# Performance work log

Measured on AMD Instinct MI355X. Metric: run time of the kernel, lower is better.

## Reference

```python
import jax, jax.numpy as jnp
import numpy as np


def _gcn_conv(x, src, dst, W, b, n_nodes):
    # PyG GCNConv: add self-loops, symmetric deg^{-1/2} normalization, then linear.
    xw = x @ W  # [N, H]
    # degree including self-loop (count of incoming edges at dst + 1)
    deg = jnp.zeros((n_nodes,), dtype=xw.dtype).at[dst].add(1.0) + 1.0
    dinv = jax.lax.rsqrt(deg)  # deg >= 1 always
    coef = (dinv[src] * dinv[dst])[:, None]  # [E, 1]
    out = jnp.zeros_like(xw).at[dst].add(xw[src] * coef)
    # self-loop edge i->i has norm dinv[i]^2
    out = out + xw * (dinv * dinv)[:, None]
    return out + b


def setup_inputs() -> dict:
    key = jax.random.key(0)
    ks = jax.random.split(key, 6)
    N, E, F, H, G = 200000, 600000, 128, 128, 64
    x = jax.random.normal(ks[0], (N, F), dtype=jnp.float32)
    edge_index = jax.random.randint(ks[1], (2, E), 0, N, dtype=jnp.int64)
    batch = jnp.sort(jax.random.randint(ks[2], (N,), 0, G, dtype=jnp.int64))
    W1 = jax.random.normal(ks[3], (F, H), dtype=jnp.float32) * (1.0 / np.sqrt(F))
    b1 = jnp.zeros((H,), dtype=jnp.float32)
    W2 = jax.random.normal(ks[4], (H, H), dtype=jnp.float32) * (1.0 / np.sqrt(H))
    b2 = jnp.zeros((H,), dtype=jnp.float32)
    return {"x": x, "edge_index": edge_index, "batch": batch, "num_graphs": G,
            "W1": W1, "b1": b1, "W2": W2, "b2": b2}


def reference(x, edge_index, batch, num_graphs, W1, b1, W2, b2):
    n_nodes = x.shape[0]
    # feature standardization (torch .std is unbiased, ddof=1)
    x = (x - x.mean(axis=0, keepdims=True)) / x.std(axis=0, keepdims=True, ddof=1)
    src, dst = edge_index[0], edge_index[1]
    h = jax.nn.relu(_gcn_conv(x, src, dst, W1, b1, n_nodes))
    # dropout p=0 -> identity
    h = jax.nn.relu(_gcn_conv(h, src, dst, W2, b2, n_nodes))
    # global_add_pool over batch ids
    return jax.ops.segment_sum(h, batch, num_segments=num_graphs)
```

## Files before the change

### kernel.cpp

```cpp
#include <hip/hip_runtime.h>

#define FDIM 128

typedef __attribute__((ext_vector_type(8))) short short8;
typedef __attribute__((ext_vector_type(4))) float f32x4;

__device__ inline unsigned short f2bf(float f) {
    unsigned int u = __float_as_uint(f);
    unsigned int r = u + 0x7FFFu + ((u >> 16) & 1u);
    return (unsigned short)(r >> 16);
}
__device__ inline float bf2f(unsigned short b) {
    return __uint_as_float((unsigned int)b << 16);
}
__device__ inline void bf8_fma(short8 v, float c, float* acc) {
#pragma unroll
    for (int k = 0; k < 8; ++k)
        acc[k] = fmaf(bf2f(((const unsigned short*)&v)[k]), c, acc[k]);
}

__global__ __launch_bounds__(256) void pre_combo(const float* __restrict__ x, int N,
                                                 float* __restrict__ partials, int statBlocks,
                                                 const int* __restrict__ dst, int E,
                                                 int* __restrict__ cnt) {
    if ((int)blockIdx.x >= statBlocks) {
        int e = (blockIdx.x - statBlocks) * 256 + threadIdx.x;
        if (e < E) atomicAdd(&cnt[dst[e]], 1);
        return;
    }
    const int c4 = threadIdx.x & 31;
    const int rg = threadIdx.x >> 5;
    float4 s = make_float4(0.f, 0.f, 0.f, 0.f);
    float4 q = make_float4(0.f, 0.f, 0.f, 0.f);
    for (long r = (long)blockIdx.x * 8 + rg; r < N; r += (long)statBlocks * 8) {
        float4 v = ((const float4*)x)[r * 32 + c4];
        s.x += v.x; s.y += v.y; s.z += v.z; s.w += v.w;
        q.x += v.x * v.x; q.y += v.y * v.y; q.z += v.z * v.z; q.w += v.w * v.w;
    }
    __shared__ float red[8][32][8];
    float* p = red[rg][c4];
    p[0] = s.x; p[1] = s.y; p[2] = s.z; p[3] = s.w;
    p[4] = q.x; p[5] = q.y; p[6] = q.z; p[7] = q.w;
    __syncthreads();
    if (rg == 0) {
#pragma unroll
        for (int g = 1; g < 8; ++g) {
            const float* o = red[g][c4];
#pragma unroll
            for (int j = 0; j < 8; ++j) red[0][c4][j] += o[j];
        }
        const float* r0 = red[0][c4];
        float* out = &partials[(size_t)blockIdx.x * 256];
        ((float4*)out)[c4] = make_float4(r0[0], r0[1], r0[2], r0[3]);
        ((float4*)(out + 128))[c4] = make_float4(r0[4], r0[5], r0[6], r0[7]);
    }
}

__global__ __launch_bounds__(256) void mid_combo(const int* __restrict__ cnt, int N,
                                                 int* __restrict__ start,
                                                 int* __restrict__ wcur,
                                                 int* __restrict__ counter,
                                                 float* __restrict__ dinv,
                                                 const float* __restrict__ partials,
                                                 int nblk, int offsBlocks,
                                                 const float* __restrict__ W1,
                                                 const float* __restrict__ W2,
                                                 unsigned short* __restrict__ WT1,
                                                 unsigned short* __restrict__ WT2,
                                                 float* __restrict__ bias0) {
    const int tid = threadIdx.x;
    if ((int)blockIdx.x < offsBlocks) {
        __shared__ int sh[256];
        __shared__ int base;
        int i = blockIdx.x * 256 + tid;
        int v = (i < N) ? cnt[i] : 0;
        sh[tid] = v;
        __syncthreads();
        for (int off = 1; off < 256; off <<= 1) {
            int t = (tid >= off) ? sh[tid - off] : 0;
            __syncthreads();
            sh[tid] += t;
            __syncthreads();
        }
        if (tid == 255) base = atomicAdd(counter, sh[255]);
        __syncthreads();
        int excl = base + sh[tid] - v;
        if (i < N) {
            start[i] = excl;
            wcur[i] = excl;
            dinv[i] = rsqrtf((float)v + 1.0f);
        }
        return;
    }
    const int b = blockIdx.x - offsBlocks;
    const int h = tid & 127;
    const int seg = tid >> 7;
    if (b < 8) {
        __shared__ float red[32][32];
        __shared__ float scol[32], mean_sh[16], rstd_sh[16];
        const int rg = tid >> 3;
        const int f = tid & 7;
        const int colbase = (f < 4) ? (b * 16 + f * 4) : (128 + b * 16 + (f - 4) * 4);
        float4 a = make_float4(0.f, 0.f, 0.f, 0.f);
        for (int row = rg; row < nblk; row += 32) {
            float4 v = *(const float4*)&partials[(size_t)row * 256 + colbase];
            a.x += v.x; a.y += v.y; a.z += v.z; a.w += v.w;
        }
        *(float4*)&red[rg][f * 4] = a;
        __syncthreads();
        if (tid < 32) {
            float s = 0.f;
#pragma unroll
            for (int r = 0; r < 32; ++r) s += red[r][tid];
            scol[tid] = s;
        }
        __syncthreads();
        if (tid < 16) {
            float m = scol[tid] / (float)N;
            float var = (scol[16 + tid] - (float)N * m * m) / (float)(N - 1);
            mean_sh[tid] = m;
            rstd_sh[tid] = rsqrtf(var);
        }
        __syncthreads();
        float acc = 0.f;
#pragma unroll
        for (int jj = 0; jj < 8; ++jj) {
            int jl = seg * 8 + jj;
            int j2 = b * 16 + jl;
            float w = W1[j2 * FDIM + h] * rstd_sh[jl];
            WT1[h * FDIM + j2] = f2bf(w);
            acc += mean_sh[jl] * w;
        }
        unsafeAtomicAdd(&bias0[h], -acc);
    } else {
#pragma unroll
        for (int jj = 0; jj < 8; ++jj) {
            int j2 = (b - 8) * 16 + seg * 8 + jj;
            WT2[h * FDIM + j2] = f2bf(W2[j2 * FDIM + h]);
        }
    }
}

__global__ __launch_bounds__(256, 4) void gemm1_fill(const float* __restrict__ A,
                                                     const unsigned short* __restrict__ WT,
                                                     const float* __restrict__ bias,
                                                     unsigned short* __restrict__ C, int M,
                                                     int gemmBlocks,
                                                     const int* __restrict__ src,
                                                     const int* __restrict__ dst,
                                                     const float* __restrict__ dinv,
                                                     int* __restrict__ wcur,
                                                     int2* __restrict__ edata, int E) {
    const int tid = threadIdx.x;
    if ((int)blockIdx.x >= gemmBlocks) {
        int e = (blockIdx.x - gemmBlocks) * 256 + tid;
        if (e < E) {
            int s = src[e], d = dst[e];
            int pos = atomicAdd(&wcur[d], 1);
            edata[pos] = make_int2(s, __float_as_int(dinv[s] * dinv[d]));
        }
        return;
    }
    constexpr int LDA = 136;
    __shared__ unsigned short Alds[64 * LDA];
    const int row0 = blockIdx.x * 64;

    for (int i = tid; i < 64 * 32; i += 256) {
        int r = i >> 5, c4 = i & 31;
        int row = row0 + r;
        float4 v = make_float4(0.f, 0.f, 0.f, 0.f);
        if (row < M) v = ((const float4*)A)[(size_t)row * 32 + c4];
        ushort4 p;
        p.x = f2bf(v.x); p.y = f2bf(v.y); p.z = f2bf(v.z); p.w = f2bf(v.w);
        *(ushort4*)&Alds[r * LDA + c4 * 4] = p;
    }
    __syncthreads();

    const int lane = tid & 63;
    const int wave = tid >> 6;
    const int m16 = lane & 15;
    const int quad = lane >> 4;

    f32x4 acc[8];
#pragma unroll
    for (int t = 0; t < 8; ++t) acc[t] = (f32x4){0.f, 0.f, 0.f, 0.f};

    const unsigned short* Abase = &Alds[(wave * 16 + m16) * LDA + quad * 8];
    const unsigned short* Wg = &WT[(size_t)m16 * FDIM + quad * 8];
#pragma unroll
    for (int s = 0; s < 4; ++s) {
        short8 a = *(const short8*)&Abase[s * 32];
#pragma unroll
        for (int t = 0; t < 8; ++t) {
            short8 b = *(const short8*)&Wg[t * 16 * FDIM + s * 32];
            acc[t] = __builtin_amdgcn_mfma_f32_16x16x32_bf16(b, a, acc[t], 0, 0, 0);
        }
    }

    const int r = row0 + wave * 16 + m16;
    if (r < M) {
#pragma unroll
        for (int t = 0; t < 8; ++t) {
            ushort4 o;
            o.x = f2bf(acc[t][0] + bias[t * 16 + quad * 4 + 0]);
            o.y = f2bf(acc[t][1] + bias[t * 16 + quad * 4 + 1]);
            o.z = f2bf(acc[t][2] + bias[t * 16 + quad * 4 + 2]);
            o.w = f2bf(acc[t][3] + bias[t * 16 + quad * 4 + 3]);
            *(ushort4*)&C[(size_t)r * FDIM + t * 16 + quad * 4] = o;
        }
    }
}

__global__ __launch_bounds__(256) void agg_gemm2(const unsigned short* __restrict__ xw,
                                                 const float* __restrict__ dinv,
                                                 const int* __restrict__ start,
                                                 const int* __restrict__ cnt,
                                                 const int2* __restrict__ edata,
                                                 const float* __restrict__ bvec,
                                                 const unsigned short* __restrict__ WT2,
                                                 unsigned short* __restrict__ out,
                                                 int N) {
    const int base = blockIdx.x * 16;
    const int node = base + (threadIdx.x >> 4);
    const int l8 = threadIdx.x & 15;
    const bool active = node < N;
    const int nidx = active ? node : (N - 1);

    float dv = dinv[nidx];
    float d2 = dv * dv;
    float4 b0 = ((const float4*)bvec)[l8 * 2];
    float4 b1v = ((const float4*)bvec)[l8 * 2 + 1];
    float acc[8] = {b0.x, b0.y, b0.z, b0.w, b1v.x, b1v.y, b1v.z, b1v.w};
    short8 sv = *(const short8*)&xw[(size_t)nidx * FDIM + l8 * 8];
    bf8_fma(sv, d2, acc);

    int j = start[nidx];
    const int s1 = j + (active ? cnt[nidx] : 0);
    for (; j + 4 <= s1; j += 4) {
        int2 e0 = edata[j], e1 = edata[j + 1], e2 = edata[j + 2], e3 = edata[j + 3];
        short8 u0 = *(const short8*)&xw[(size_t)e0.x * FDIM + l8 * 8];
        short8 u1 = *(const short8*)&xw[(size_t)e1.x * FDIM + l8 * 8];
        short8 u2 = *(const short8*)&xw[(size_t)e2.x * FDIM + l8 * 8];
        short8 u3 = *(const short8*)&xw[(size_t)e3.x * FDIM + l8 * 8];
        bf8_fma(u0, __int_as_float(e0.y), acc);
        bf8_fma(u1, __int_as_float(e1.y), acc);
        bf8_fma(u2, __int_as_float(e2.y), acc);
        bf8_fma(u3, __int_as_float(e3.y), acc);
    }
    for (; j < s1; ++j) {
        int2 ed = edata[j];
        short8 u = *(const short8*)&xw[(size_t)ed.x * FDIM + l8 * 8];
        bf8_fma(u, __int_as_float(ed.y), acc);
    }

    constexpr int LDH = 136;
    __shared__ unsigned short hlds[16 * LDH];
    {
        ushort4 o0, o1;
        if (active) {
            o0.x = f2bf(fmaxf(acc[0], 0.f)); o0.y = f2bf(fmaxf(acc[1], 0.f));
            o0.z = f2bf(fmaxf(acc[2], 0.f)); o0.w = f2bf(fmaxf(acc[3], 0.f));
            o1.x = f2bf(fmaxf(acc[4], 0.f)); o1.y = f2bf(fmaxf(acc[5], 0.f));
            o1.z = f2bf(fmaxf(acc[6], 0.f)); o1.w = f2bf(fmaxf(acc[7], 0.f));
        } else {
            o0.x = 0; o0.y = 0; o0.z = 0; o0.w = 0;
            o1.x = 0; o1.y = 0; o1.z = 0; o1.w = 0;
        }
        unsigned short* hp = &hlds[(threadIdx.x >> 4) * LDH + l8 * 8];
        *(ushort4*)hp = o0;
        *(ushort4*)(hp + 4) = o1;
    }
    __syncthreads();

    const int lane = threadIdx.x & 63;
    const int wave = threadIdx.x >> 6;
    const int m16 = lane & 15;
    const int quad = lane >> 4;
    f32x4 c0 = (f32x4){0.f, 0.f, 0.f, 0.f};
    f32x4 c1 = (f32x4){0.f, 0.f, 0.f, 0.f};
    const unsigned short* Abase = &hlds[m16 * LDH + quad * 8];
    const unsigned short* Wg = &WT2[(size_t)(wave * 32 + m16) * FDIM + quad * 8];
#pragma unroll
    for (int s = 0; s < 4; ++s) {
        short8 a = *(const short8*)&Abase[s * 32];
        short8 w0 = *(const short8*)&Wg[s * 32];
        short8 w1 = *(const short8*)&Wg[16 * FDIM + s * 32];
        c0 = __builtin_amdgcn_mfma_f32_16x16x32_bf16(w0, a, c0, 0, 0, 0);
        c1 = __builtin_amdgcn_mfma_f32_16x16x32_bf16(w1, a, c1, 0, 0, 0);
    }
    const int r = base + m16;
    if (r < N) {
        ushort4 o;
        o.x = f2bf(c0[0]); o.y = f2bf(c0[1]); o.z = f2bf(c0[2]); o.w = f2bf(c0[3]);
        *(ushort4*)&out[(size_t)r * FDIM + wave * 32 + quad * 4] = o;
        o.x = f2bf(c1[0]); o.y = f2bf(c1[1]); o.z = f2bf(c1[2]); o.w = f2bf(c1[3]);
        *(ushort4*)&out[(size_t)r * FDIM + wave * 32 + 16 + quad * 4] = o;
    }
}

template <bool POOL>
__global__ __launch_bounds__(256) void aggregate(const unsigned short* __restrict__ xw,
                                                 const float* __restrict__ dinv,
                                                 const int* __restrict__ start,
                                                 const int* __restrict__ cnt,
                                                 const int2* __restrict__ edata,
                                                 const float* __restrict__ bvec,
                                                 unsigned short* __restrict__ out,
                                                 const int* __restrict__ batch,
                                                 float* __restrict__ pool_part,
                                                 int* __restrict__ ptag,
                                                 float* __restrict__ pooled, int N) {
    const int base = blockIdx.x * 16;
    const int node = base + (threadIdx.x >> 4);
    const int l8 = threadIdx.x & 15;
    const bool active = node < N;
    if (!POOL && !active) return;
    const int nidx = active ? node : (N - 1);

    float dv = dinv[nidx];
    float d2 = dv * dv;
    float4 b0 = ((const float4*)bvec)[l8 * 2];
    float4 b1 = ((const float4*)bvec)[l8 * 2 + 1];
    float acc[8] = {b0.x, b0.y, b0.z, b0.w, b1.x, b1.y, b1.z, b1.w};
    short8 sv = *(const short8*)&xw[(size_t)nidx * FDIM + l8 * 8];
    bf8_fma(sv, d2, acc);

    int j = start[nidx];
    const int s1 = j + (active ? cnt[nidx] : 0);
    for (; j + 4 <= s1; j += 4) {
        int2 e0 = edata[j], e1 = edata[j + 1], e2 = edata[j + 2], e3 = edata[j + 3];
        short8 u0 = *(const short8*)&xw[(size_t)e0.x * FDIM + l8 * 8];
        short8 u1 = *(const short8*)&xw[(size_t)e1.x * FDIM + l8 * 8];
        short8 u2 = *(const short8*)&xw[(size_t)e2.x * FDIM + l8 * 8];
        short8 u3 = *(const short8*)&xw[(size_t)e3.x * FDIM + l8 * 8];
        bf8_fma(u0, __int_as_float(e0.y), acc);
        bf8_fma(u1, __int_as_float(e1.y), acc);
        bf8_fma(u2, __int_as_float(e2.y), acc);
        bf8_fma(u3, __int_as_float(e3.y), acc);
    }
    for (; j < s1; ++j) {
        int2 ed = edata[j];
        short8 u = *(const short8*)&xw[(size_t)ed.x * FDIM + l8 * 8];
        bf8_fma(u, __int_as_float(ed.y), acc);
    }

    if constexpr (!POOL) {
        short8 o;
#pragma unroll
        for (int k = 0; k < 8; ++k)
            ((unsigned short*)&o)[k] = f2bf(fmaxf(acc[k], 0.f));
        *(short8*)&out[(size_t)node * FDIM + l8 * 8] = o;
    } else {
        float r[8];
#pragma unroll
        for (int k = 0; k < 8; ++k) r[k] = active ? fmaxf(acc[k], 0.f) : 0.f;
        int g0 = batch[base];
        int g1 = batch[min(base + 15, N - 1)];
        if (g0 == g1) {
            __shared__ float red[16][FDIM];
            float* dst = &red[threadIdx.x >> 4][l8 * 8];
            *(float4*)dst = make_float4(r[0], r[1], r[2], r[3]);
            *(float4*)(dst + 4) = make_float4(r[4], r[5], r[6], r[7]);
            __syncthreads();
            if (threadIdx.x < FDIM) {
                float s = 0.f;
#pragma unroll
                for (int i = 0; i < 16; ++i) s += red[i][threadIdx.x];
                pool_part[(size_t)blockIdx.x * FDIM + threadIdx.x] = s;
                if (threadIdx.x == 0) ptag[blockIdx.x] = g0;
            }
        } else {
            if (threadIdx.x == 0) ptag[blockIdx.x] = -1;
            if (active) {
                int g = batch[node];
#pragma unroll
                for (int k = 0; k < 8; ++k)
                    unsafeAtomicAdd(&pooled[g * FDIM + l8 * 8 + k], r[k]);
            }
        }
    }
}

__global__ __launch_bounds__(128) void pool_reduce(const float* __restrict__ pool_part,
                                                   const int* __restrict__ ptag,
                                                   int nslots, float* __restrict__ out) {
    int per = (nslots + gridDim.x - 1) / gridDim.x;
    int s0 = blockIdx.x * per;
    int s1 = min(s0 + per, nslots);
    int t = threadIdx.x;
    float acc = 0.f;
    int cur = -1;
    for (int s = s0; s < s1; ++s) {
        int g = ptag[s];
        if (g < 0) continue;
        if (g != cur) {
            if (cur >= 0) unsafeAtomicAdd(&out[cur * FDIM + t], acc);
            acc = 0.f;
            cur = g;
        }
        acc += pool_part[(size_t)s * FDIM + t];
    }
    if (cur >= 0) unsafeAtomicAdd(&out[cur * FDIM + t], acc);
}

extern "C" void kernel_launch(void* const* d_in, const int* in_sizes, int n_in,
                              void* d_out, int out_size, void* d_ws, size_t ws_size,
                              hipStream_t stream) {
    const float* x = (const float*)d_in[0];
    const int* ei = (const int*)d_in[1];
    const int* batch = (const int*)d_in[2];
    const float* W1 = (const float*)d_in[4];
    const float* b1 = (const float*)d_in[5];
    const float* W2 = (const float*)d_in[6];
    const float* b2 = (const float*)d_in[7];

    const int N = in_sizes[2];
    const int E = in_sizes[1] / 2;
    const int* srcp = ei;
    const int* dstp = ei + E;

    const size_t NF = (size_t)N * FDIM;
    const int aggGrid = (N + 15) / 16;
    unsigned short* bufA = (unsigned short*)d_ws;
    unsigned short* bufB = bufA + NF;
    int* cnt = (int*)(bufB + NF);
    int* counter = cnt + N;
    float* bias0 = (float*)(counter + 4);
    float* dinv = bias0 + FDIM;
    int* start = (int*)(dinv + N);
    int* wcur = start + N;
    unsigned short* WT1 = (unsigned short*)(wcur + N);
    unsigned short* WT2 = WT1 + FDIM * FDIM;
    int2* edata = (int2*)(WT2 + FDIM * FDIM);
    float* pool_part = (float*)(edata + E);
    int* ptag = (int*)(pool_part + (size_t)aggGrid * FDIM);
    float* partials = (float*)edata;
    const int STAT_BLOCKS = 512;

    hipMemsetAsync(cnt, 0, ((size_t)N + 4 + FDIM) * sizeof(int), stream);
    hipMemsetAsync(d_out, 0, (size_t)out_size * sizeof(float), stream);

    const int degBlocks = (E + 255) / 256;
    const int offsBlocks = (N + 255) / 256;
    const int gemmGrid = (N + 63) / 64;

    pre_combo<<<STAT_BLOCKS + degBlocks, 256, 0, stream>>>(x, N, partials, STAT_BLOCKS,
                                                           dstp, E, cnt);
    mid_combo<<<offsBlocks + 16, 256, 0, stream>>>(cnt, N, start, wcur, counter, dinv,
                                                   partials, STAT_BLOCKS, offsBlocks,
                                                   W1, W2, WT1, WT2, bias0);

    gemm1_fill<<<gemmGrid + degBlocks, 256, 0, stream>>>(x, WT1, bias0, bufA, N, gemmGrid,
                                                         srcp, dstp, dinv, wcur, edata, E);

    agg_gemm2<<<aggGrid, 256, 0, stream>>>(bufA, dinv, start, cnt, edata, b1, WT2,
                                           bufB, N);

    aggregate<true><<<aggGrid, 256, 0, stream>>>(bufB, dinv, start, cnt, edata, b2,
                                                 nullptr, batch, pool_part, ptag,
                                                 (float*)d_out, N);
    pool_reduce<<<256, 128, 0, stream>>>(pool_part, ptag, aggGrid, (float*)d_out);
}
```

Measured before the change: 433.6 us.

## Emit bf16 copy of x in stats pass and stage weights in LDS for GEMM1

The statistics kernel now writes a bf16 copy of x as it reads it, so the first GEMM reads half the bytes instead of re-reading fp32 x. GEMM1 also stages the transposed weight matrix into shared memory rather than loading B fragments from global memory, and drops the occupancy hint in launch bounds. This trades an extra 51 MB write in the stats pass plus roughly 50 KB of LDS per block (lower occupancy) for a smaller read in GEMM1 and on-chip weight reuse.

```diff
diff --git a/kernel.cpp b/kernel.cpp
--- a/kernel.cpp
+++ b/kernel.cpp
@@ -22,7 +22,8 @@
 __global__ __launch_bounds__(256) void pre_combo(const float* __restrict__ x, int N,
                                                  float* __restrict__ partials, int statBlocks,
                                                  const int* __restrict__ dst, int E,
-                                                 int* __restrict__ cnt) {
+                                                 int* __restrict__ cnt,
+                                                 unsigned short* __restrict__ xbf) {
     if ((int)blockIdx.x >= statBlocks) {
         int e = (blockIdx.x - statBlocks) * 256 + threadIdx.x;
         if (e < E) atomicAdd(&cnt[dst[e]], 1);
@@ -36,6 +37,9 @@
         float4 v = ((const float4*)x)[r * 32 + c4];
         s.x += v.x; s.y += v.y; s.z += v.z; s.w += v.w;
         q.x += v.x * v.x; q.y += v.y * v.y; q.z += v.z * v.z; q.w += v.w * v.w;
+        ushort4 p;
+        p.x = f2bf(v.x); p.y = f2bf(v.y); p.z = f2bf(v.z); p.w = f2bf(v.w);
+        ((ushort4*)xbf)[r * 32 + c4] = p;
     }
     __shared__ float red[8][32][8];
     float* p = red[rg][c4];
@@ -141,16 +145,16 @@
     }
 }
 
-__global__ __launch_bounds__(256, 4) void gemm1_fill(const float* __restrict__ A,
-                                                     const unsigned short* __restrict__ WT,
-                                                     const float* __restrict__ bias,
-                                                     unsigned short* __restrict__ C, int M,
-                                                     int gemmBlocks,
-                                                     const int* __restrict__ src,
-                                                     const int* __restrict__ dst,
-                                                     const float* __restrict__ dinv,
-                                                     int* __restrict__ wcur,
-                                                     int2* __restrict__ edata, int E) {
+__global__ __launch_bounds__(256) void gemm1_fill(const unsigned short* __restrict__ A,
+                                                  const unsigned short* __restrict__ WT,
+                                                  const float* __restrict__ bias,
+                                                  unsigned short* __restrict__ C, int M,
+                                                  int gemmBlocks,
+                                                  const int* __restrict__ src,
+                                                  const int* __restrict__ dst,
+                                                  const float* __restrict__ dinv,
+                                                  int* __restrict__ wcur,
+                                                  int2* __restrict__ edata, int E) {
     const int tid = threadIdx.x;
     if ((int)blockIdx.x >= gemmBlocks) {
         int e = (blockIdx.x - gemmBlocks) * 256 + tid;
@@ -163,16 +167,19 @@
     }
     constexpr int LDA = 136;
     __shared__ unsigned short Alds[64 * LDA];
+    __shared__ unsigned short Wlds[FDIM * LDA];
     const int row0 = blockIdx.x * 64;
 
-    for (int i = tid; i < 64 * 32; i += 256) {
-        int r = i >> 5, c4 = i & 31;
+    for (int i = tid; i < FDIM * 16; i += 256) {
+        int r = i >> 4, g = i & 15;
+        *(int4*)&Wlds[r * LDA + g * 8] = *(const int4*)&WT[r * FDIM + g * 8];
+    }
+    for (int i = tid; i < 64 * 16; i += 256) {
+        int r = i >> 4, g = i & 15;
         int row = row0 + r;
-        float4 v = make_float4(0.f, 0.f, 0.f, 0.f);
-        if (row < M) v = ((const float4*)A)[(size_t)row * 32 + c4];
-        ushort4 p;
-        p.x = f2bf(v.x); p.y = f2bf(v.y); p.z = f2bf(v.z); p.w = f2bf(v.w);
-        *(ushort4*)&Alds[r * LDA + c4 * 4] = p;
+        int4 v = make_int4(0, 0, 0, 0);
+        if (row < M) v = *(const int4*)&A[(size_t)row * FDIM + g * 8];
+        *(int4*)&Alds[r * LDA + g * 8] = v;
     }
     __syncthreads();
 
@@ -186,13 +193,13 @@
     for (int t = 0; t < 8; ++t) acc[t] = (f32x4){0.f, 0.f, 0.f, 0.f};
 
     const unsigned short* Abase = &Alds[(wave * 16 + m16) * LDA + quad * 8];
-    const unsigned short* Wg = &WT[(size_t)m16 * FDIM + quad * 8];
+    const unsigned short* Wbase = &Wlds[m16 * LDA + quad * 8];
 #pragma unroll
     for (int s = 0; s < 4; ++s) {
         short8 a = *(const short8*)&Abase[s * 32];
 #pragma unroll
         for (int t = 0; t < 8; ++t) {
-            short8 b = *(const short8*)&Wg[t * 16 * FDIM + s * 32];
+            short8 b = *(const short8*)&Wbase[t * 16 * LDA + s * 32];
             acc[t] = __builtin_amdgcn_mfma_f32_16x16x32_bf16(b, a, acc[t], 0, 0, 0);
         }
     }
@@ -445,13 +452,14 @@
     const int gemmGrid = (N + 63) / 64;
 
     pre_combo<<<STAT_BLOCKS + degBlocks, 256, 0, stream>>>(x, N, partials, STAT_BLOCKS,
-                                                           dstp, E, cnt);
+                                                           dstp, E, cnt, bufB);
     mid_combo<<<offsBlocks + 16, 256, 0, stream>>>(cnt, N, start, wcur, counter, dinv,
                                                    partials, STAT_BLOCKS, offsBlocks,
                                                    W1, W2, WT1, WT2, bias0);
 
-    gemm1_fill<<<gemmGrid + degBlocks, 256, 0, stream>>>(x, WT1, bias0, bufA, N, gemmGrid,
-                                                         srcp, dstp, dinv, wcur, edata, E);
+    gemm1_fill<<<gemmGrid + degBlocks, 256, 0, stream>>>(bufB, WT1, bias0, bufA, N,
+                                                         gemmGrid, srcp, dstp, dinv,
+                                                         wcur, edata, E);
 
     agg_gemm2<<<aggGrid, 256, 0, stream>>>(bufA, dinv, start, cnt, edata, b1, WT2,
                                            bufB, N);
```

New measurement: 409.7 us. -5.5%, faster.
